# Kernel tuning notes

Measured on AMD Instinct MI355X. Metric: run time of the kernel, lower is better.

Reference implementation:

```python
import jax, jax.numpy as jnp
import numpy as np

D = 128
SCALE = 1.0 / np.sqrt(D).astype(np.float32)


def setup_inputs() -> dict:
    key = jax.random.key(0)
    kq, kk, kv = jax.random.split(key, 3)
    B, L = 16, 2048
    q = jax.random.normal(kq, (B, L, D), dtype=jnp.float32)
    k = jax.random.normal(kk, (B, L, D), dtype=jnp.float32)
    v = jax.random.normal(kv, (B, L, D), dtype=jnp.float32)
    return {"q": q, "k": k, "v": v}


def reference(q, k, v):
    # attention[b, i, j] = sum_d q[b,i,d] * k[b,j,d], scaled
    scores = jnp.einsum('bqd,bkd->bqk', q, k) * SCALE
    attention = jax.nn.softmax(scores, axis=2)
    # dropout p=0.0 -> identity
    context = jnp.einsum('bqk,bkd->bqd', attention, v)
    return (context, attention)
```

## Files before the change

### kernel.cpp

```cpp
#include <hip/hip_runtime.h>
#include <hip/hip_bf16.h>

#define NB 16
#define NL 2048
#define ND 128
#define QSCALE 0.08838834764831845f
#define QSCALE2 (0.08838834764831845f * 1.4426950408889634f)

using short8 = __attribute__((ext_vector_type(8))) short;
using f32x4  = __attribute__((ext_vector_type(4))) float;

__device__ __forceinline__ float hw_exp2(float x) {
  return __builtin_amdgcn_exp2f(x);
}

__device__ __forceinline__ unsigned short bfr(float f) {
  unsigned u = __float_as_uint(f);
  unsigned r = u + 0x7FFFu + ((u >> 16) & 1u);
  return (unsigned short)(r >> 16);
}
__device__ __forceinline__ float bf2f(unsigned short h) {
  return __uint_as_float(((unsigned)h) << 16);
}
__device__ __forceinline__ unsigned pk(float a, float b) {
  return (unsigned)bfr(a) | ((unsigned)bfr(b) << 16);
}

typedef const __attribute__((address_space(1))) unsigned int* gas1_t;
typedef __attribute__((address_space(3))) unsigned int* las3_t;
__device__ __forceinline__ void async_lds16(const unsigned short* g, unsigned short* l) {
  __builtin_amdgcn_global_load_lds((gas1_t)g, (las3_t)l, 16, 0, 0);
}

__device__ __forceinline__ short8 swz_frag(const unsigned short* base, int row, int chunk) {
  return *(const short8*)(base + row * 128 + (((chunk ^ (row & 7)) << 3)));
}

#define WS_KB 0
#define WS_VT 8388608
#define WS_LINV 16777216
#define WS_NEED 16908288

__global__ __launch_bounds__(256)
void prep_k(const float* __restrict__ kg, unsigned short* __restrict__ Kb) {
  size_t base = ((size_t)blockIdx.x * 256 + threadIdx.x) * 4;
  float4 x = *(const float4*)(kg + base);
  ushort4 o;
  o.x = bfr(x.x); o.y = bfr(x.y); o.z = bfr(x.z); o.w = bfr(x.w);
  *(ushort4*)(Kb + base) = o;
}

__global__ __launch_bounds__(256)
void prep_vt(const float* __restrict__ vg, unsigned short* __restrict__ Vt) {
  __shared__ float T[32][129];
  const int b = blockIdx.y, j0 = blockIdx.x * 32, tid = threadIdx.x;
  const float* vb = vg + ((size_t)b * NL + j0) * ND;
#pragma unroll
  for (int r = 0; r < 4; ++r) {
    int f4 = tid + r * 256;
    int j  = f4 >> 5;
    int c4 = f4 & 31;
    float4 x = *(const float4*)(vb + (size_t)j * ND + c4 * 4);
    T[j][c4 * 4 + 0] = x.x; T[j][c4 * 4 + 1] = x.y;
    T[j][c4 * 4 + 2] = x.z; T[j][c4 * 4 + 3] = x.w;
  }
  __syncthreads();
  const int d = tid >> 1, h = tid & 1;
  unsigned short* orow = Vt + ((size_t)b * ND + d) * NL + j0 + h * 16;
#pragma unroll
  for (int g = 0; g < 4; ++g) {
    ushort4 o;
    o.x = bfr(T[h * 16 + g * 4 + 0][d]);
    o.y = bfr(T[h * 16 + g * 4 + 1][d]);
    o.z = bfr(T[h * 16 + g * 4 + 2][d]);
    o.w = bfr(T[h * 16 + g * 4 + 3][d]);
    *(ushort4*)(orow + g * 4) = o;
  }
}

__device__ __forceinline__ void load_q_frags(const float* qrow, int quad,
                                             short8* qh, short8* ql, float scale) {
#pragma unroll
  for (int kk = 0; kk < 4; ++kk) {
    const float* p = qrow + kk * 32 + quad * 8;
    float4 x = *(const float4*)(p);
    float4 y = *(const float4*)(p + 4);
    float e[8] = {x.x, x.y, x.z, x.w, y.x, y.y, y.z, y.w};
    short8 th, tl;
#pragma unroll
    for (int t = 0; t < 8; ++t) {
      float qs = e[t] * scale;
      unsigned short h = bfr(qs);
      th[t] = (short)h;
      tl[t] = (short)bfr(qs - bf2f(h));
    }
    qh[kk] = th;
    ql[kk] = tl;
  }
}

__global__ __launch_bounds__(256, 2)
void attn_ctx(const float* __restrict__ q, const unsigned short* __restrict__ Kb,
              const unsigned short* __restrict__ Vt,
              float* __restrict__ ctx, float* __restrict__ linv_ws) {
  __shared__ unsigned short KsL[128 * 128];
  __shared__ unsigned short VsL[128 * 128];
  __shared__ unsigned short Ps[4][16][36];

  const int b    = blockIdx.y;
  const int i0   = blockIdx.x * 64;
  const int tid  = threadIdx.x;
  const int wave = tid >> 6;
  const int lane = tid & 63;
  const int quad = lane >> 4;
  const int l16  = lane & 15;

  const float* qrow = q + ((size_t)b * NL + i0 + wave * 16 + l16) * ND;
  short8 qh[4], ql[4];
  load_q_frags(qrow, quad, qh, ql, QSCALE2);

  f32x4 oacc[8];
#pragma unroll
  for (int i = 0; i < 8; ++i) oacc[i] = (f32x4){0.f, 0.f, 0.f, 0.f};
  float lsum = 0.f;

  const unsigned short* kbb = Kb + (size_t)b * NL * ND;
  const unsigned short* vtb = Vt + (size_t)b * ND * NL;

  for (int j0 = 0; j0 < NL; j0 += 128) {
    __syncthreads();
#pragma unroll
    for (int r = 0; r < 8; ++r) {
      int row = wave * 4 + r * 16 + (lane >> 4);
      int c   = lane & 15;
      async_lds16(kbb + (size_t)(j0 + row) * ND + ((c ^ (row & 7)) << 3),
                  KsL + (wave * 64 + r * 256) * 8);
    }
#pragma unroll
    for (int r = 0; r < 8; ++r) {
      int d = wave * 4 + r * 16 + (lane >> 4);
      int c = lane & 15;
      async_lds16(vtb + (size_t)d * NL + j0 + ((c ^ (d & 7)) << 3),
                  VsL + (wave * 64 + r * 256) * 8);
    }
    __syncthreads();

#pragma unroll
    for (int ks = 0; ks < 4; ++ks) {
      f32x4 a0 = {0.f, 0.f, 0.f, 0.f}, a1 = {0.f, 0.f, 0.f, 0.f};
#pragma unroll
      for (int kk = 0; kk < 4; ++kk) {
        short8 k0 = swz_frag(KsL, ks * 32 + l16, kk * 4 + quad);
        short8 k1 = swz_frag(KsL, ks * 32 + 16 + l16, kk * 4 + quad);
        a0 = __builtin_amdgcn_mfma_f32_16x16x32_bf16(k0, qh[kk], a0, 0, 0, 0);
        a0 = __builtin_amdgcn_mfma_f32_16x16x32_bf16(k0, ql[kk], a0, 0, 0, 0);
        a1 = __builtin_amdgcn_mfma_f32_16x16x32_bf16(k1, qh[kk], a1, 0, 0, 0);
        a1 = __builtin_amdgcn_mfma_f32_16x16x32_bf16(k1, ql[kk], a1, 0, 0, 0);
      }
      float e0[4], e1[4];
#pragma unroll
      for (int r = 0; r < 4; ++r) {
        e0[r] = hw_exp2(a0[r]);
        e1[r] = hw_exp2(a1[r]);
        lsum += e0[r] + e1[r];
      }
      uint2 w0, w1;
      w0.x = pk(e0[0], e0[1]); w0.y = pk(e0[2], e0[3]);
      w1.x = pk(e1[0], e1[1]); w1.y = pk(e1[2], e1[3]);
      *(uint2*)&Ps[wave][l16][quad * 4]      = w0;
      *(uint2*)&Ps[wave][l16][16 + quad * 4] = w1;
      short8 pa = *(const short8*)&Ps[wave][l16][quad * 8];
#pragma unroll
      for (int dt = 0; dt < 8; ++dt) {
        short8 vf = swz_frag(VsL, dt * 16 + l16, ks * 4 + quad);
        oacc[dt] = __builtin_amdgcn_mfma_f32_16x16x32_bf16(pa, vf, oacc[dt], 0, 0, 0);
      }
    }
  }

  lsum += __shfl_xor(lsum, 16);
  lsum += __shfl_xor(lsum, 32);
  float sinv = 1.0f / lsum;
  if (lane < 16)
    linv_ws[(size_t)b * NL + i0 + wave * 16 + lane] = sinv;

#pragma unroll
  for (int r = 0; r < 4; ++r) {
    float lir = __shfl(sinv, quad * 4 + r, 16);
    float* crow = ctx + ((size_t)b * NL + i0 + wave * 16 + quad * 4 + r) * ND;
#pragma unroll
    for (int dt = 0; dt < 8; ++dt)
      crow[dt * 16 + l16] = oacc[dt][r] * lir;
  }
}

__global__ __launch_bounds__(256, 4)
void attn_probs(const float* __restrict__ q, const unsigned short* __restrict__ Kb,
                const float* __restrict__ linv_ws, float* __restrict__ attn) {
  __shared__ unsigned short KsL[128 * 128];

  const int b    = blockIdx.z;
  const int i0   = blockIdx.y * 64;
  const int j0   = blockIdx.x * 128;
  const int tid  = threadIdx.x;
  const int wave = tid >> 6;
  const int lane = tid & 63;
  const int quad = lane >> 4;
  const int l16  = lane & 15;
  const int row0 = i0 + wave * 16;

  const unsigned short* kbb = Kb + (size_t)b * NL * ND;
#pragma unroll
  for (int r = 0; r < 8; ++r) {
    int row = wave * 4 + r * 16 + (lane >> 4);
    int c   = lane & 15;
    async_lds16(kbb + (size_t)(j0 + row) * ND + ((c ^ (row & 7)) << 3),
                KsL + (wave * 64 + r * 256) * 8);
  }

  const float* qrow = q + ((size_t)b * NL + row0 + l16) * ND;
  short8 qh[4], ql[4];
  load_q_frags(qrow, quad, qh, ql, QSCALE2);
  float li = linv_ws[(size_t)b * NL + row0 + l16];

  __syncthreads();

#pragma unroll
  for (int jg = 0; jg < 8; ++jg) {
    f32x4 a = {0.f, 0.f, 0.f, 0.f};
#pragma unroll
    for (int kk = 0; kk < 4; ++kk) {
      short8 kf = swz_frag(KsL, jg * 16 + l16, kk * 4 + quad);
      a = __builtin_amdgcn_mfma_f32_16x16x32_bf16(kf, qh[kk], a, 0, 0, 0);
      a = __builtin_amdgcn_mfma_f32_16x16x32_bf16(kf, ql[kk], a, 0, 0, 0);
    }
    f32x4 o;
#pragma unroll
    for (int r = 0; r < 4; ++r) o[r] = hw_exp2(a[r]) * li;
    *(f32x4*)(attn + ((size_t)b * NL + row0 + l16) * NL + j0 + jg * 16 + quad * 4) = o;
  }
}

__global__ __launch_bounds__(256, 2)
void attn_fused(const float* __restrict__ q, const float* __restrict__ kg,
                const float* __restrict__ vg, float* __restrict__ out) {
  float* ctx  = out;
  float* attn = out + (size_t)NB * NL * ND;
  const int b    = blockIdx.y;
  const int i0   = blockIdx.x * 64;
  const int tid  = threadIdx.x;
  const int wave = tid >> 6;
  const int lane = tid & 63;
  const int quad = lane >> 4;
  const int l16  = lane & 15;

  __shared__ short Ksf[32][136];
  __shared__ short Vtf[128][40];
  __shared__ short Ps2[4][16][40];

  const float* qrow = q + ((size_t)b * NL + i0 + wave * 16 + l16) * ND;
  short8 qh[4], ql[4];
  load_q_frags(qrow, quad, qh, ql, QSCALE);

  f32x4 oacc[8];
#pragma unroll
  for (int i = 0; i < 8; ++i) oacc[i] = (f32x4){0.f, 0.f, 0.f, 0.f};
  float lsum[4] = {0.f, 0.f, 0.f, 0.f};

  const float* kb = kg + (size_t)b * NL * ND;
  const float* vb = vg + (size_t)b * NL * ND;

  for (int j0 = 0; j0 < NL; j0 += 32) {
    __syncthreads();
#pragma unroll
    for (int rr = 0; rr < 4; ++rr) {
      int idx = tid + rr * 256;
      int row = idx >> 5;
      int c4  = idx & 31;
      float4 kv = *(const float4*)(kb + (size_t)(j0 + row) * ND + c4 * 4);
      ushort4 ks;
      ks.x = bfr(kv.x); ks.y = bfr(kv.y); ks.z = bfr(kv.z); ks.w = bfr(kv.w);
      *(ushort4*)&Ksf[row][c4 * 4] = ks;
      float4 vv = *(const float4*)(vb + (size_t)(j0 + row) * ND + c4 * 4);
      Vtf[c4 * 4 + 0][row] = (short)bfr(vv.x);
      Vtf[c4 * 4 + 1][row] = (short)bfr(vv.y);
      Vtf[c4 * 4 + 2][row] = (short)bfr(vv.z);
      Vtf[c4 * 4 + 3][row] = (short)bfr(vv.w);
    }
    __syncthreads();

    f32x4 a0 = {0.f, 0.f, 0.f, 0.f}, a1 = {0.f, 0.f, 0.f, 0.f};
#pragma unroll
    for (int kk = 0; kk < 4; ++kk) {
      short8 k0 = *(const short8*)&Ksf[l16][kk * 32 + quad * 8];
      short8 k1 = *(const short8*)&Ksf[l16 + 16][kk * 32 + quad * 8];
      a0 = __builtin_amdgcn_mfma_f32_16x16x32_bf16(qh[kk], k0, a0, 0, 0, 0);
      a0 = __builtin_amdgcn_mfma_f32_16x16x32_bf16(ql[kk], k0, a0, 0, 0, 0);
      a1 = __builtin_amdgcn_mfma_f32_16x16x32_bf16(qh[kk], k1, a1, 0, 0, 0);
      a1 = __builtin_amdgcn_mfma_f32_16x16x32_bf16(ql[kk], k1, a1, 0, 0, 0);
    }
#pragma unroll
    for (int r = 0; r < 4; ++r) {
      float e0 = __expf(a0[r]);
      float e1 = __expf(a1[r]);
      lsum[r] += e0 + e1;
      Ps2[wave][quad * 4 + r][l16]      = (short)bfr(e0);
      Ps2[wave][quad * 4 + r][l16 + 16] = (short)bfr(e1);
    }
    __syncthreads();
    short8 pa = *(const short8*)&Ps2[wave][l16][quad * 8];
#pragma unroll
    for (int dt = 0; dt < 8; ++dt) {
      short8 vf = *(const short8*)&Vtf[dt * 16 + l16][quad * 8];
      oacc[dt] = __builtin_amdgcn_mfma_f32_16x16x32_bf16(pa, vf, oacc[dt], 0, 0, 0);
    }
  }

  float linv[4];
#pragma unroll
  for (int r = 0; r < 4; ++r) {
    float s = lsum[r];
    s += __shfl_xor(s, 1, 16);
    s += __shfl_xor(s, 2, 16);
    s += __shfl_xor(s, 4, 16);
    s += __shfl_xor(s, 8, 16);
    linv[r] = 1.0f / s;
  }
#pragma unroll
  for (int r = 0; r < 4; ++r) {
    float* crow = ctx + ((size_t)b * NL + i0 + wave * 16 + quad * 4 + r) * ND;
#pragma unroll
    for (int dt = 0; dt < 8; ++dt)
      crow[dt * 16 + l16] = oacc[dt][r] * linv[r];
  }

  for (int j0 = 0; j0 < NL; j0 += 32) {
    __syncthreads();
#pragma unroll
    for (int rr = 0; rr < 4; ++rr) {
      int idx = tid + rr * 256;
      int row = idx >> 5;
      int c4  = idx & 31;
      float4 kv = *(const float4*)(kb + (size_t)(j0 + row) * ND + c4 * 4);
      ushort4 ks;
      ks.x = bfr(kv.x); ks.y = bfr(kv.y); ks.z = bfr(kv.z); ks.w = bfr(kv.w);
      *(ushort4*)&Ksf[row][c4 * 4] = ks;
    }
    __syncthreads();
    f32x4 a0 = {0.f, 0.f, 0.f, 0.f}, a1 = {0.f, 0.f, 0.f, 0.f};
#pragma unroll
    for (int kk = 0; kk < 4; ++kk) {
      short8 k0 = *(const short8*)&Ksf[l16][kk * 32 + quad * 8];
      short8 k1 = *(const short8*)&Ksf[l16 + 16][kk * 32 + quad * 8];
      a0 = __builtin_amdgcn_mfma_f32_16x16x32_bf16(qh[kk], k0, a0, 0, 0, 0);
      a0 = __builtin_amdgcn_mfma_f32_16x16x32_bf16(ql[kk], k0, a0, 0, 0, 0);
      a1 = __builtin_amdgcn_mfma_f32_16x16x32_bf16(qh[kk], k1, a1, 0, 0, 0);
      a1 = __builtin_amdgcn_mfma_f32_16x16x32_bf16(ql[kk], k1, a1, 0, 0, 0);
    }
    float* arow = attn + ((size_t)b * NL + i0 + wave * 16 + quad * 4) * NL + j0;
#pragma unroll
    for (int r = 0; r < 4; ++r) {
      arow[(size_t)r * NL + l16]      = __expf(a0[r]) * linv[r];
      arow[(size_t)r * NL + l16 + 16] = __expf(a1[r]) * linv[r];
    }
  }
}

extern "C" void kernel_launch(void* const* d_in, const int* in_sizes, int n_in,
                              void* d_out, int out_size, void* d_ws, size_t ws_size,
                              hipStream_t stream) {
  const float* q = (const float*)d_in[0];
  const float* k = (const float*)d_in[1];
  const float* v = (const float*)d_in[2];
  float* out = (float*)d_out;

  if (ws_size >= (size_t)WS_NEED) {
    unsigned short* Kb = (unsigned short*)((char*)d_ws + WS_KB);
    unsigned short* Vt = (unsigned short*)((char*)d_ws + WS_VT);
    float* linv        = (float*)((char*)d_ws + WS_LINV);
    float* ctx  = out;
    float* attn = out + (size_t)NB * NL * ND;

    prep_k<<<dim3(4096), dim3(256), 0, stream>>>(k, Kb);
    prep_vt<<<dim3(64, 16), dim3(256), 0, stream>>>(v, Vt);
    attn_ctx<<<dim3(32, 16), dim3(256), 0, stream>>>(q, Kb, Vt, ctx, linv);
    attn_probs<<<dim3(16, 32, 16), dim3(256), 0, stream>>>(q, Kb, linv, attn);
  } else {
    dim3 grid(NL / 64, NB);
    attn_fused<<<grid, dim3(256), 0, stream>>>(q, k, v, out);
  }
}
```

Baseline: 399.3 us.

## Double-buffer K/V tiles in attn_ctx and widen attn_probs row tile

```diff
diff --git a/kernel.cpp b/kernel.cpp
--- a/kernel.cpp
+++ b/kernel.cpp
@@ -32,8 +32,9 @@
   __builtin_amdgcn_global_load_lds((gas1_t)g, (las3_t)l, 16, 0, 0);
 }
 
-__device__ __forceinline__ short8 swz_frag(const unsigned short* base, int row, int chunk) {
-  return *(const short8*)(base + row * 128 + (((chunk ^ (row & 7)) << 3)));
+__device__ __forceinline__ short8 swz_frag_s(const unsigned short* base, int row,
+                                             int chunk, int stride) {
+  return *(const short8*)(base + row * stride + ((chunk ^ (row & 7)) << 3));
 }
 
 #define WS_KB 0
@@ -103,8 +104,8 @@
 void attn_ctx(const float* __restrict__ q, const unsigned short* __restrict__ Kb,
               const unsigned short* __restrict__ Vt,
               float* __restrict__ ctx, float* __restrict__ linv_ws) {
-  __shared__ unsigned short KsL[128 * 128];
-  __shared__ unsigned short VsL[128 * 128];
+  __shared__ unsigned short KsD[2][64 * 128];
+  __shared__ unsigned short VsD[2][128 * 64];
   __shared__ unsigned short Ps[4][16][36];
 
   const int b    = blockIdx.y;
@@ -115,6 +116,9 @@
   const int quad = lane >> 4;
   const int l16  = lane & 15;
 
+  const unsigned short* kbb = Kb + (size_t)b * NL * ND;
+  const unsigned short* vtb = Vt + (size_t)b * ND * NL;
+
   const float* qrow = q + ((size_t)b * NL + i0 + wave * 16 + l16) * ND;
   short8 qh[4], ql[4];
   load_q_frags(qrow, quad, qh, ql, QSCALE2);
@@ -124,34 +128,37 @@
   for (int i = 0; i < 8; ++i) oacc[i] = (f32x4){0.f, 0.f, 0.f, 0.f};
   float lsum = 0.f;
 
-  const unsigned short* kbb = Kb + (size_t)b * NL * ND;
-  const unsigned short* vtb = Vt + (size_t)b * ND * NL;
-
-  for (int j0 = 0; j0 < NL; j0 += 128) {
-    __syncthreads();
-#pragma unroll
-    for (int r = 0; r < 8; ++r) {
-      int row = wave * 4 + r * 16 + (lane >> 4);
+  auto stage = [&](int buf, int j0) {
+#pragma unroll
+    for (int r = 0; r < 4; ++r) {
+      int row = r * 16 + wave * 4 + (lane >> 4);
       int c   = lane & 15;
       async_lds16(kbb + (size_t)(j0 + row) * ND + ((c ^ (row & 7)) << 3),
-                  KsL + (wave * 64 + r * 256) * 8);
-    }
-#pragma unroll
-    for (int r = 0; r < 8; ++r) {
-      int d = wave * 4 + r * 16 + (lane >> 4);
-      int c = lane & 15;
-      async_lds16(vtb + (size_t)d * NL + j0 + ((c ^ (d & 7)) << 3),
-                  VsL + (wave * 64 + r * 256) * 8);
-    }
-    __syncthreads();
-
-#pragma unroll
-    for (int ks = 0; ks < 4; ++ks) {
+                  &KsD[buf][r * 2048 + wave * 512]);
+    }
+#pragma unroll
+    for (int r = 0; r < 4; ++r) {
+      int row = r * 32 + wave * 8 + (lane >> 3);
+      int c   = lane & 7;
+      async_lds16(vtb + (size_t)row * NL + j0 + ((c ^ (row & 7)) << 3),
+                  &VsD[buf][r * 2048 + wave * 512]);
+    }
+  };
+
+  stage(0, 0);
+  __syncthreads();
+
+  int cur = 0;
+  for (int t = 0; t < NL / 64; ++t) {
+    if (t + 1 < NL / 64) stage(cur ^ 1, (t + 1) * 64);
+
+#pragma unroll
+    for (int ks = 0; ks < 2; ++ks) {
       f32x4 a0 = {0.f, 0.f, 0.f, 0.f}, a1 = {0.f, 0.f, 0.f, 0.f};
 #pragma unroll
       for (int kk = 0; kk < 4; ++kk) {
-        short8 k0 = swz_frag(KsL, ks * 32 + l16, kk * 4 + quad);
-        short8 k1 = swz_frag(KsL, ks * 32 + 16 + l16, kk * 4 + quad);
+        short8 k0 = swz_frag_s(KsD[cur], ks * 32 + l16, kk * 4 + quad, 128);
+        short8 k1 = swz_frag_s(KsD[cur], ks * 32 + 16 + l16, kk * 4 + quad, 128);
         a0 = __builtin_amdgcn_mfma_f32_16x16x32_bf16(k0, qh[kk], a0, 0, 0, 0);
         a0 = __builtin_amdgcn_mfma_f32_16x16x32_bf16(k0, ql[kk], a0, 0, 0, 0);
         a1 = __builtin_amdgcn_mfma_f32_16x16x32_bf16(k1, qh[kk], a1, 0, 0, 0);
@@ -172,10 +179,12 @@
       short8 pa = *(const short8*)&Ps[wave][l16][quad * 8];
 #pragma unroll
       for (int dt = 0; dt < 8; ++dt) {
-        short8 vf = swz_frag(VsL, dt * 16 + l16, ks * 4 + quad);
+        short8 vf = swz_frag_s(VsD[cur], dt * 16 + l16, ks * 4 + quad, 64);
         oacc[dt] = __builtin_amdgcn_mfma_f32_16x16x32_bf16(pa, vf, oacc[dt], 0, 0, 0);
       }
     }
+    __syncthreads();
+    cur ^= 1;
   }
 
   lsum += __shfl_xor(lsum, 16);
@@ -200,7 +209,7 @@
   __shared__ unsigned short KsL[128 * 128];
 
   const int b    = blockIdx.z;
-  const int i0   = blockIdx.y * 64;
+  const int i0   = blockIdx.y * 128;
   const int j0   = blockIdx.x * 128;
   const int tid  = threadIdx.x;
   const int wave = tid >> 6;
@@ -208,6 +217,7 @@
   const int quad = lane >> 4;
   const int l16  = lane & 15;
   const int row0 = i0 + wave * 16;
+  const int row1 = i0 + 64 + wave * 16;
 
   const unsigned short* kbb = Kb + (size_t)b * NL * ND;
 #pragma unroll
@@ -218,26 +228,34 @@
                 KsL + (wave * 64 + r * 256) * 8);
   }
 
-  const float* qrow = q + ((size_t)b * NL + row0 + l16) * ND;
-  short8 qh[4], ql[4];
-  load_q_frags(qrow, quad, qh, ql, QSCALE2);
-  float li = linv_ws[(size_t)b * NL + row0 + l16];
+  short8 qh0[4], ql0[4], qh1[4], ql1[4];
+  load_q_frags(q + ((size_t)b * NL + row0 + l16) * ND, quad, qh0, ql0, QSCALE2);
+  load_q_frags(q + ((size_t)b * NL + row1 + l16) * ND, quad, qh1, ql1, QSCALE2);
+  float li0 = linv_ws[(size_t)b * NL + row0 + l16];
+  float li1 = linv_ws[(size_t)b * NL + row1 + l16];
 
   __syncthreads();
 
 #pragma unroll
   for (int jg = 0; jg < 8; ++jg) {
-    f32x4 a = {0.f, 0.f, 0.f, 0.f};
+    f32x4 a0 = {0.f, 0.f, 0.f, 0.f};
+    f32x4 a1 = {0.f, 0.f, 0.f, 0.f};
 #pragma unroll
     for (int kk = 0; kk < 4; ++kk) {
-      short8 kf = swz_frag(KsL, jg * 16 + l16, kk * 4 + quad);
-      a = __builtin_amdgcn_mfma_f32_16x16x32_bf16(kf, qh[kk], a, 0, 0, 0);
-      a = __builtin_amdgcn_mfma_f32_16x16x32_bf16(kf, ql[kk], a, 0, 0, 0);
-    }
-    f32x4 o;
-#pragma unroll
-    for (int r = 0; r < 4; ++r) o[r] = hw_exp2(a[r]) * li;
-    *(f32x4*)(attn + ((size_t)b * NL + row0 + l16) * NL + j0 + jg * 16 + quad * 4) = o;
+      short8 kf = swz_frag_s(KsL, jg * 16 + l16, kk * 4 + quad, 128);
+      a0 = __builtin_amdgcn_mfma_f32_16x16x32_bf16(kf, qh0[kk], a0, 0, 0, 0);
+      a0 = __builtin_amdgcn_mfma_f32_16x16x32_bf16(kf, ql0[kk], a0, 0, 0, 0);
+      a1 = __builtin_amdgcn_mfma_f32_16x16x32_bf16(kf, qh1[kk], a1, 0, 0, 0);
+      a1 = __builtin_amdgcn_mfma_f32_16x16x32_bf16(kf, ql1[kk], a1, 0, 0, 0);
+    }
+    f32x4 o0, o1;
+#pragma unroll
+    for (int r = 0; r < 4; ++r) {
+      o0[r] = hw_exp2(a0[r]) * li0;
+      o1[r] = hw_exp2(a1[r]) * li1;
+    }
+    *(f32x4*)(attn + ((size_t)b * NL + row0 + l16) * NL + j0 + jg * 16 + quad * 4) = o0;
+    *(f32x4*)(attn + ((size_t)b * NL + row1 + l16) * NL + j0 + jg * 16 + quad * 4) = o1;
   }
 }
 
@@ -384,7 +402,7 @@
     prep_k<<<dim3(4096), dim3(256), 0, stream>>>(k, Kb);
     prep_vt<<<dim3(64, 16), dim3(256), 0, stream>>>(v, Vt);
     attn_ctx<<<dim3(32, 16), dim3(256), 0, stream>>>(q, Kb, Vt, ctx, linv);
-    attn_probs<<<dim3(16, 32, 16), dim3(256), 0, stream>>>(q, Kb, linv, attn);
+    attn_probs<<<dim3(16, 16, 16), dim3(256), 0, stream>>>(q, Kb, linv, attn);
   } else {
     dim3 grid(NL / 64, NB);
     attn_fused<<<grid, dim3(256), 0, stream>>>(q, k, v, out);
```

Result: slower. 446.0 us (+11.7%).

## Store unnormalized bf16 probabilities during context pass and rescale in a separate kernel

Applied to the files above, without the earlier changes.

```diff
diff --git a/kernel.cpp b/kernel.cpp
--- a/kernel.cpp
+++ b/kernel.cpp
@@ -33,13 +33,15 @@
 }
 
 __device__ __forceinline__ short8 swz_frag(const unsigned short* base, int row, int chunk) {
-  return *(const short8*)(base + row * 128 + (((chunk ^ (row & 7)) << 3)));
+  return *(const short8*)(base + row * 128 + ((chunk ^ (row & 7)) << 3));
 }
 
 #define WS_KB 0
 #define WS_VT 8388608
 #define WS_LINV 16777216
+#define WS_P 16908288
 #define WS_NEED 16908288
+#define WS_NEED_P (16908288 + 134217728)
 
 __global__ __launch_bounds__(256)
 void prep_k(const float* __restrict__ kg, unsigned short* __restrict__ Kb) {
@@ -99,10 +101,12 @@
   }
 }
 
+template <int WP>
 __global__ __launch_bounds__(256, 2)
 void attn_ctx(const float* __restrict__ q, const unsigned short* __restrict__ Kb,
               const unsigned short* __restrict__ Vt,
-              float* __restrict__ ctx, float* __restrict__ linv_ws) {
+              float* __restrict__ ctx, float* __restrict__ linv_ws,
+              unsigned short* __restrict__ P_ws) {
   __shared__ unsigned short KsL[128 * 128];
   __shared__ unsigned short VsL[128 * 128];
   __shared__ unsigned short Ps[4][16][36];
@@ -126,6 +130,8 @@
 
   const unsigned short* kbb = Kb + (size_t)b * NL * ND;
   const unsigned short* vtb = Vt + (size_t)b * ND * NL;
+  unsigned short* prow =
+      WP ? P_ws + ((size_t)b * NL + i0 + wave * 16 + l16) * NL + quad * 8 : nullptr;
 
   for (int j0 = 0; j0 < NL; j0 += 128) {
     __syncthreads();
@@ -170,6 +176,9 @@
       *(uint2*)&Ps[wave][l16][quad * 4]      = w0;
       *(uint2*)&Ps[wave][l16][16 + quad * 4] = w1;
       short8 pa = *(const short8*)&Ps[wave][l16][quad * 8];
+      if (WP) {
+        *(short8*)(prow + j0 + ks * 32) = pa;
+      }
 #pragma unroll
       for (int dt = 0; dt < 8; ++dt) {
         short8 vf = swz_frag(VsL, dt * 16 + l16, ks * 4 + quad);
@@ -192,6 +201,27 @@
     for (int dt = 0; dt < 8; ++dt)
       crow[dt * 16 + l16] = oacc[dt][r] * lir;
   }
+}
+
+__global__ __launch_bounds__(256)
+void probs_scale(const unsigned short* __restrict__ P, const float* __restrict__ linv_ws,
+                 float* __restrict__ attn) {
+  const size_t row = blockIdx.x;
+  const float li = linv_ws[row];
+  const int c = threadIdx.x * 8;
+  short8 p = *(const short8*)(P + row * NL + c);
+  float4 o0, o1;
+  o0.x = bf2f((unsigned short)p[0]) * li;
+  o0.y = bf2f((unsigned short)p[1]) * li;
+  o0.z = bf2f((unsigned short)p[2]) * li;
+  o0.w = bf2f((unsigned short)p[3]) * li;
+  o1.x = bf2f((unsigned short)p[4]) * li;
+  o1.y = bf2f((unsigned short)p[5]) * li;
+  o1.z = bf2f((unsigned short)p[6]) * li;
+  o1.w = bf2f((unsigned short)p[7]) * li;
+  float* a = attn + row * NL + c;
+  *(float4*)a = o0;
+  *(float4*)(a + 4) = o1;
 }
 
 __global__ __launch_bounds__(256, 4)
@@ -383,8 +413,15 @@
 
     prep_k<<<dim3(4096), dim3(256), 0, stream>>>(k, Kb);
     prep_vt<<<dim3(64, 16), dim3(256), 0, stream>>>(v, Vt);
-    attn_ctx<<<dim3(32, 16), dim3(256), 0, stream>>>(q, Kb, Vt, ctx, linv);
-    attn_probs<<<dim3(16, 32, 16), dim3(256), 0, stream>>>(q, Kb, linv, attn);
+
+    if (ws_size >= (size_t)WS_NEED_P) {
+      unsigned short* Pws = (unsigned short*)((char*)d_ws + WS_P);
+      attn_ctx<1><<<dim3(32, 16), dim3(256), 0, stream>>>(q, Kb, Vt, ctx, linv, Pws);
+      probs_scale<<<dim3(NB * NL), dim3(256), 0, stream>>>(Pws, linv, attn);
+    } else {
+      attn_ctx<0><<<dim3(32, 16), dim3(256), 0, stream>>>(q, Kb, Vt, ctx, linv, nullptr);
+      attn_probs<<<dim3(16, 32, 16), dim3(256), 0, stream>>>(q, Kb, linv, attn);
+    }
   } else {
     dim3 grid(NL / 64, NB);
     attn_fused<<<grid, dim3(256), 0, stream>>>(q, k, v, out);
```

Result: slower. 408.6 us (+2.4%).

## Stash unnormalized bf16 probabilities from ctx pass, rescale in place instead of recomputing

Applied to the files above, without the earlier changes.

```diff
diff --git a/kernel.cpp b/kernel.cpp
--- a/kernel.cpp
+++ b/kernel.cpp
@@ -33,7 +33,7 @@
 }
 
 __device__ __forceinline__ short8 swz_frag(const unsigned short* base, int row, int chunk) {
-  return *(const short8*)(base + row * 128 + (((chunk ^ (row & 7)) << 3)));
+  return *(const short8*)(base + row * 128 + ((chunk ^ (row & 7)) << 3));
 }
 
 #define WS_KB 0
@@ -102,7 +102,8 @@
 __global__ __launch_bounds__(256, 2)
 void attn_ctx(const float* __restrict__ q, const unsigned short* __restrict__ Kb,
               const unsigned short* __restrict__ Vt,
-              float* __restrict__ ctx, float* __restrict__ linv_ws) {
+              float* __restrict__ ctx, float* __restrict__ linv_ws,
+              float* __restrict__ attn) {
   __shared__ unsigned short KsL[128 * 128];
   __shared__ unsigned short VsL[128 * 128];
   __shared__ unsigned short Ps[4][16][36];
@@ -126,6 +127,8 @@
 
   const unsigned short* kbb = Kb + (size_t)b * NL * ND;
   const unsigned short* vtb = Vt + (size_t)b * ND * NL;
+  unsigned short* prow =
+      (unsigned short*)(attn + ((size_t)b * NL + i0 + wave * 16 + l16) * NL) + quad * 8;
 
   for (int j0 = 0; j0 < NL; j0 += 128) {
     __syncthreads();
@@ -170,6 +173,7 @@
       *(uint2*)&Ps[wave][l16][quad * 4]      = w0;
       *(uint2*)&Ps[wave][l16][16 + quad * 4] = w1;
       short8 pa = *(const short8*)&Ps[wave][l16][quad * 8];
+      *(short8*)(prow + j0 + ks * 32) = pa;
 #pragma unroll
       for (int dt = 0; dt < 8; ++dt) {
         short8 vf = swz_frag(VsL, dt * 16 + l16, ks * 4 + quad);
@@ -194,50 +198,28 @@
   }
 }
 
-__global__ __launch_bounds__(256, 4)
-void attn_probs(const float* __restrict__ q, const unsigned short* __restrict__ Kb,
-                const float* __restrict__ linv_ws, float* __restrict__ attn) {
-  __shared__ unsigned short KsL[128 * 128];
-
-  const int b    = blockIdx.z;
-  const int i0   = blockIdx.y * 64;
-  const int j0   = blockIdx.x * 128;
-  const int tid  = threadIdx.x;
-  const int wave = tid >> 6;
-  const int lane = tid & 63;
-  const int quad = lane >> 4;
-  const int l16  = lane & 15;
-  const int row0 = i0 + wave * 16;
-
-  const unsigned short* kbb = Kb + (size_t)b * NL * ND;
-#pragma unroll
-  for (int r = 0; r < 8; ++r) {
-    int row = wave * 4 + r * 16 + (lane >> 4);
-    int c   = lane & 15;
-    async_lds16(kbb + (size_t)(j0 + row) * ND + ((c ^ (row & 7)) << 3),
-                KsL + (wave * 64 + r * 256) * 8);
-  }
-
-  const float* qrow = q + ((size_t)b * NL + row0 + l16) * ND;
-  short8 qh[4], ql[4];
-  load_q_frags(qrow, quad, qh, ql, QSCALE2);
-  float li = linv_ws[(size_t)b * NL + row0 + l16];
-
-  __syncthreads();
-
-#pragma unroll
-  for (int jg = 0; jg < 8; ++jg) {
-    f32x4 a = {0.f, 0.f, 0.f, 0.f};
-#pragma unroll
-    for (int kk = 0; kk < 4; ++kk) {
-      short8 kf = swz_frag(KsL, jg * 16 + l16, kk * 4 + quad);
-      a = __builtin_amdgcn_mfma_f32_16x16x32_bf16(kf, qh[kk], a, 0, 0, 0);
-      a = __builtin_amdgcn_mfma_f32_16x16x32_bf16(kf, ql[kk], a, 0, 0, 0);
-    }
-    f32x4 o;
-#pragma unroll
-    for (int r = 0; r < 4; ++r) o[r] = hw_exp2(a[r]) * li;
-    *(f32x4*)(attn + ((size_t)b * NL + row0 + l16) * NL + j0 + jg * 16 + quad * 4) = o;
+__global__ __launch_bounds__(256)
+void probs_scale(float* __restrict__ attn, const float* __restrict__ linv_ws) {
+  const int t = threadIdx.x;
+#pragma unroll
+  for (int rr = 0; rr < 8; ++rr) {
+    const size_t row = (size_t)blockIdx.x * 8 + rr;
+    const float li = linv_ws[row];
+    float* arow = attn + row * NL;
+    short8 p = *(const short8*)((const unsigned short*)arow + t * 8);
+    asm volatile("s_waitcnt vmcnt(0)" ::: "memory");
+    __syncthreads();
+    float4 o0, o1;
+    o0.x = bf2f((unsigned short)p[0]) * li;
+    o0.y = bf2f((unsigned short)p[1]) * li;
+    o0.z = bf2f((unsigned short)p[2]) * li;
+    o0.w = bf2f((unsigned short)p[3]) * li;
+    o1.x = bf2f((unsigned short)p[4]) * li;
+    o1.y = bf2f((unsigned short)p[5]) * li;
+    o1.z = bf2f((unsigned short)p[6]) * li;
+    o1.w = bf2f((unsigned short)p[7]) * li;
+    *(float4*)(arow + t * 8) = o0;
+    *(float4*)(arow + t * 8 + 4) = o1;
   }
 }
 
@@ -383,8 +365,8 @@
 
     prep_k<<<dim3(4096), dim3(256), 0, stream>>>(k, Kb);
     prep_vt<<<dim3(64, 16), dim3(256), 0, stream>>>(v, Vt);
-    attn_ctx<<<dim3(32, 16), dim3(256), 0, stream>>>(q, Kb, Vt, ctx, linv);
-    attn_probs<<<dim3(16, 32, 16), dim3(256), 0, stream>>>(q, Kb, linv, attn);
+    attn_ctx<<<dim3(32, 16), dim3(256), 0, stream>>>(q, Kb, Vt, ctx, linv, attn);
+    probs_scale<<<dim3(NB * NL / 8), dim3(256), 0, stream>>>(attn, linv);
   } else {
     dim3 grid(NL / 64, NB);
     attn_fused<<<grid, dim3(256), 0, stream>>>(q, k, v, out);
```

After: 430.8 us. 1.08x slower.
